# Performance work log

Hardware: AMD Instinct MI355X
Metric: run time of the kernel (lower is better)

The kernel has to match this reference:

```python
import jax, jax.numpy as jnp
import numpy as np

GAMMA = 10.0

def setup_inputs() -> dict:
    key = jax.random.key(0)
    B, N, D = 9, 4096, 2048
    # scale so gamma * squared pairwise distances is O(1) (mimics normalized features)
    x = jax.random.normal(key, (B, N, D), dtype=jnp.float32) * 0.01
    return {"x": x}

def reference(x):
    # x: [B, N, D]; pairwise per-sample squared distances via the GEMM identity
    # ||a-b||^2 = ||a||^2 + ||b||^2 - 2<a,b>
    B = x.shape[0]
    s = jnp.sum(x * x, axis=-1)                      # [B, N]
    dots = jnp.einsum('ind,jnd->ijn', x, x)          # [B, B, N]
    sq = jnp.maximum(s[:, None, :] + s[None, :, :] - 2.0 * dots, 0.0)  # [B, B, N]
    snm = jnp.mean(jnp.exp(-GAMMA * sq), axis=-1)    # [B, B]
    snm = jnp.where(jnp.eye(B, dtype=bool), 0.0, snm)  # i != j only
    direct_div = jnp.sum(snm)
    det_div = -jnp.linalg.det(snm)
    sign, logabs = jnp.linalg.slogdet(snm)
    # torch.logdet returns NaN for non-positive determinant
    logdet_div = -jnp.where(sign > 0, logabs, jnp.nan)
    return (direct_div, det_div, logdet_div)
```

## Files before the change

### kernel.cpp

```cpp
#include <hip/hip_runtime.h>
#include <math.h>

#define BB 9
#define NN 4096
#define DD 2048
#define NPAIR 45
#define NOFF 36
#define WSCOL 64


__global__ void zero_ws_kernel(float* __restrict__ ws) {
    int t = blockIdx.x * blockDim.x + threadIdx.x;
    if (t < NOFF * WSCOL) ws[t] = 0.0f;
}

__global__ __launch_bounds__(256, 4) void pairdot_kernel(const float* __restrict__ x,
                                                         float* __restrict__ ws) {
    const int tid = threadIdx.x;
    const int wave = tid >> 6;
    const int lane = tid & 63;
    const int n = blockIdx.x * 4 + wave;

    float acc[NPAIR];
#pragma unroll
    for (int p = 0; p < NPAIR; ++p) acc[p] = 0.0f;

    const size_t rowstride = (size_t)NN * DD;
    const float* base = x + (size_t)n * DD + (size_t)(lane * 4);

#pragma unroll 1
    for (int c = 0; c < 8; ++c) {
        float4 v[BB];
#pragma unroll
        for (int i = 0; i < BB; ++i) {
            v[i] = *(const float4*)(base + (size_t)i * rowstride + c * 256);
        }
        int p = 0;
#pragma unroll
        for (int i = 0; i < BB; ++i) {
#pragma unroll
            for (int j = i; j < BB; ++j) {
                acc[p] += v[i].x * v[j].x + v[i].y * v[j].y
                        + v[i].z * v[j].z + v[i].w * v[j].w;
                ++p;
            }
        }
    }

#pragma unroll
    for (int p = 0; p < NPAIR; ++p) {
        float a = acc[p];
#pragma unroll
        for (int m = 32; m >= 1; m >>= 1) a += __shfl_xor(a, m, 64);
        acc[p] = a;
    }

    __shared__ float sums[4][NOFF];
    if (lane == 0) {
        int q = 0;
        int p = 0;
#pragma unroll
        for (int i = 0; i < BB; ++i) {
            const int di = i * BB - i * (i - 1) / 2;
            ++p;
#pragma unroll
            for (int j = i + 1; j < BB; ++j) {
                const int dj = j * BB - j * (j - 1) / 2;
                float sq = acc[di] + acc[dj] - 2.0f * acc[p];
                sq = fmaxf(sq, 0.0f);
                sums[wave][q] = __expf(-10.0f * sq);
                ++q; ++p;
            }
        }
    }
    __syncthreads();
    if (tid < NOFF) {
        float t = sums[0][tid] + sums[1][tid] + sums[2][tid] + sums[3][tid];
        atomicAdd(&ws[tid * WSCOL + (blockIdx.x & (WSCOL - 1))], t);
    }
}

__global__ __launch_bounds__(256, 1) void finalize_kernel(const float* __restrict__ ws,
                                                          float* __restrict__ out) {
    const int tid = threadIdx.x;
    const int wave = tid >> 6;
    const int lane = tid & 63;

    __shared__ float snm_f[NOFF];
#pragma unroll 1
    for (int t = 0; t < 9; ++t) {
        const int q = wave * 9 + t;
        float s = ws[q * WSCOL + lane];
#pragma unroll
        for (int m = 32; m >= 1; m >>= 1) s += __shfl_xor(s, m, 64);
        if (lane == 0) snm_f[q] = s;
    }
    __syncthreads();

    __shared__ double A[BB * BB];
    __shared__ double Fs[BB];
    __shared__ int piv_s;

    const double inv_n = 1.0 / (double)NN;
    if (tid < BB * BB) {
        const int r = tid / BB, c = tid % BB;
        if (r == c) {
            A[tid] = 0.0;
        } else {
            const int i = r < c ? r : c;
            const int j = r < c ? c : r;
            const int q = i * (2 * BB - 1 - i) / 2 + (j - i - 1);
            A[tid] = (double)snm_f[q] * inv_n;
        }
    }
    __syncthreads();

    double direct = 0.0, detv = 1.0;
    if (tid == 0) {
        for (int q = 0; q < NOFF; ++q) direct += (double)snm_f[q];
        direct = 2.0 * direct * inv_n;
    }

    for (int k = 0; k < BB; ++k) {
        if (tid == 0) {
            int piv = k;
            double mx = fabs(A[k * BB + k]);
            for (int r = k + 1; r < BB; ++r) {
                double a = fabs(A[r * BB + k]);
                if (a > mx) { mx = a; piv = r; }
            }
            piv_s = piv;
        }
        __syncthreads();
        const int piv = piv_s;
        double tk = 0.0, tp = 0.0;
        if (tid < BB) { tk = A[k * BB + tid]; tp = A[piv * BB + tid]; }
        __syncthreads();
        if (tid < BB) { A[k * BB + tid] = tp; A[piv * BB + tid] = tk; }
        __syncthreads();
        if (tid == 0) {
            detv *= A[k * BB + k];
            if (piv != k) detv = -detv;
        }
        if (tid > k && tid < BB) Fs[tid] = A[tid * BB + k] / A[k * BB + k];
        __syncthreads();
        if (tid < BB * BB) {
            const int r = tid / BB, c = tid % BB;
            if (r > k && c >= k) A[tid] -= Fs[r] * A[k * BB + c];
        }
        __syncthreads();
    }

    if (tid == 0) {
        out[0] = (float)direct;
        out[1] = (float)(-detv);
        out[2] = (detv > 0.0) ? (float)(-log(detv))
                              : __builtin_nanf("");
    }
}

extern "C" void kernel_launch(void* const* d_in, const int* in_sizes, int n_in,
                              void* d_out, int out_size, void* d_ws, size_t ws_size,
                              hipStream_t stream) {
    const float* x = (const float*)d_in[0];
    float* out = (float*)d_out;
    float* ws = (float*)d_ws;

    zero_ws_kernel<<<(NOFF * WSCOL + 255) / 256, 256, 0, stream>>>(ws);
    pairdot_kernel<<<NN / 4, 256, 0, stream>>>(x, ws);
    finalize_kernel<<<1, 256, 0, stream>>>(ws, out);
}
```

Before: 427.4 us.

## Stage rows through LDS with direct global-to-LDS loads, one block per column

```diff
diff --git a/kernel.cpp b/kernel.cpp
--- a/kernel.cpp
+++ b/kernel.cpp
@@ -7,7 +7,11 @@
 #define NPAIR 45
 #define NOFF 36
 #define WSCOL 64
+#define CHUNK 1024
 
+
+typedef const __attribute__((address_space(1))) void* as1_t;
+typedef __attribute__((address_space(3))) void* as3_t;
 
 __global__ void zero_ws_kernel(float* __restrict__ ws) {
     int t = blockIdx.x * blockDim.x + threadIdx.x;
@@ -19,22 +23,33 @@
     const int tid = threadIdx.x;
     const int wave = tid >> 6;
     const int lane = tid & 63;
-    const int n = blockIdx.x * 4 + wave;
+    const int n = blockIdx.x;
+
+    __shared__ float smem[BB][CHUNK];
+    __shared__ float psum[4][NPAIR];
+    __shared__ float dotv[NPAIR];
+
+    const size_t rowstride = (size_t)NN * DD;
 
     float acc[NPAIR];
 #pragma unroll
     for (int p = 0; p < NPAIR; ++p) acc[p] = 0.0f;
 
-    const size_t rowstride = (size_t)NN * DD;
-    const float* base = x + (size_t)n * DD + (size_t)(lane * 4);
+#pragma unroll 1
+    for (int c = 0; c < DD / CHUNK; ++c) {
+        if (c) __syncthreads();
+        const float* g0 = x + (size_t)n * DD + c * CHUNK + wave * 256 + lane * 4;
+#pragma unroll
+        for (int i = 0; i < BB; ++i) {
+            __builtin_amdgcn_global_load_lds((as1_t)(g0 + (size_t)i * rowstride),
+                                             (as3_t)&smem[i][wave * 256],
+                                             16, 0, 0);
+        }
+        __syncthreads();
 
-#pragma unroll 1
-    for (int c = 0; c < 8; ++c) {
         float4 v[BB];
 #pragma unroll
-        for (int i = 0; i < BB; ++i) {
-            v[i] = *(const float4*)(base + (size_t)i * rowstride + c * 256);
-        }
+        for (int i = 0; i < BB; ++i) v[i] = *(const float4*)&smem[i][tid * 4];
         int p = 0;
 #pragma unroll
         for (int i = 0; i < BB; ++i) {
@@ -54,29 +69,27 @@
         for (int m = 32; m >= 1; m >>= 1) a += __shfl_xor(a, m, 64);
         acc[p] = a;
     }
-
-    __shared__ float sums[4][NOFF];
+    if (lane < NPAIR) psum[wave][lane] = acc[lane];
     if (lane == 0) {
-        int q = 0;
-        int p = 0;
 #pragma unroll
-        for (int i = 0; i < BB; ++i) {
-            const int di = i * BB - i * (i - 1) / 2;
-            ++p;
-#pragma unroll
-            for (int j = i + 1; j < BB; ++j) {
-                const int dj = j * BB - j * (j - 1) / 2;
-                float sq = acc[di] + acc[dj] - 2.0f * acc[p];
-                sq = fmaxf(sq, 0.0f);
-                sums[wave][q] = __expf(-10.0f * sq);
-                ++q; ++p;
-            }
-        }
+        for (int p = 0; p < NPAIR; ++p) psum[wave][p] = acc[p];
     }
     __syncthreads();
+
+    if (tid < NPAIR) {
+        dotv[tid] = psum[0][tid] + psum[1][tid] + psum[2][tid] + psum[3][tid];
+    }
+    __syncthreads();
+
     if (tid < NOFF) {
-        float t = sums[0][tid] + sums[1][tid] + sums[2][tid] + sums[3][tid];
-        atomicAdd(&ws[tid * WSCOL + (blockIdx.x & (WSCOL - 1))], t);
+        int q = tid, i = 0;
+        while (q >= BB - 1 - i) { q -= BB - 1 - i; ++i; }
+        const int j = i + 1 + q;
+        const int pii = i * BB - i * (i - 1) / 2;
+        const int pjj = j * BB - j * (j - 1) / 2;
+        const int pij = pii + (j - i);
+        float sq = fmaxf(dotv[pii] + dotv[pjj] - 2.0f * dotv[pij], 0.0f);
+        atomicAdd(&ws[tid * WSCOL + (n & (WSCOL - 1))], __expf(-10.0f * sq));
     }
 }
 
@@ -167,6 +180,6 @@
     float* ws = (float*)d_ws;
 
     zero_ws_kernel<<<(NOFF * WSCOL + 255) / 256, 256, 0, stream>>>(ws);
-    pairdot_kernel<<<NN / 4, 256, 0, stream>>>(x, ws);
+    pairdot_kernel<<<NN, 256, 0, stream>>>(x, ws);
     finalize_kernel<<<1, 256, 0, stream>>>(ws, out);
 }
```

Measured after the change: 465.1 us. +8.8%, slower.
